# Optimization experiments

Measured on AMD Instinct MI355X. Metric: run time of the kernel, lower is better.

The kernel has to match this reference:

```python
import jax, jax.numpy as jnp
import numpy as np

NB_COMP = 8
LAT_DIM = 512
NB_NEUR = 1024
OUT_DIM = 512
N_SAMPLES = 16384


def setup_inputs() -> dict:
    key = jax.random.key(0)
    ks = jax.random.split(key, 8)
    s1 = 1.0 / np.sqrt(LAT_DIM)
    s2 = 1.0 / np.sqrt(NB_NEUR)
    return {
        "epsilon": jax.random.normal(ks[0], (N_SAMPLES, LAT_DIM), dtype=jnp.float32),
        "comp_idx": jax.random.randint(ks[1], (N_SAMPLES,), 0, NB_COMP, dtype=jnp.int32),
        "mu": jnp.zeros((NB_COMP, LAT_DIM), dtype=jnp.float32),
        "rho": jnp.zeros((NB_COMP,), dtype=jnp.float32),  # sigma = softplus(rho)
        "W1": jax.random.normal(ks[2], (NB_COMP, LAT_DIM, NB_NEUR), dtype=jnp.float32) * s1,
        "b1": jax.random.normal(ks[3], (NB_COMP, NB_NEUR), dtype=jnp.float32) * s1,
        "W2": jax.random.normal(ks[4], (NB_COMP, NB_NEUR, OUT_DIM), dtype=jnp.float32) * s2,
        "b2": jax.random.normal(ks[5], (NB_COMP, OUT_DIM), dtype=jnp.float32) * s2,
    }


def reference(epsilon, comp_idx, mu, rho, W1, b1, W2, b2):
    # GNNens.forward: per-sample categorical component dispatch through a
    # 1-hidden-layer sigmoid MLP. Vectorized as compute-all-components + select.
    sigma = jax.nn.softplus(rho)                          # [C]
    # lat_c[c,n,d] = epsilon[n,d] * sigma[c] + mu[c,d]
    lat = epsilon[None, :, :] * sigma[:, None, None] + mu[:, None, :]  # [C,N,D]
    h = jax.nn.sigmoid(jnp.einsum('cnd,cdh->cnh', lat, W1) + b1[:, None, :])  # [C,N,H]
    y = jnp.einsum('cnh,cho->cno', h, W2) + b2[:, None, :]                    # [C,N,O]
    # select each sample's routed component
    idx = comp_idx[None, :, None].astype(jnp.int32)       # [1,N,1]
    out = jnp.take_along_axis(y, idx, axis=0)[0]          # [N,O]
    return out
```

## Files before the change

kernel.cpp:

```cpp
#include <hip/hip_runtime.h>
#include <stdint.h>

#define NCOMP 8
#define LATD  512
#define HID   1024
#define OUTD  512
#define NS    16384

typedef unsigned short u16;
typedef __bf16 bf16x8 __attribute__((ext_vector_type(8)));
typedef float  f32x4  __attribute__((ext_vector_type(4)));

#define MAPS       (NS/128 + NCOMP)
#define SLOT_CHUNK ((MAPS + 7)/8)

#define ORDER_OFF  2048
#define APACK_OFF  (ORDER_OFF + NS*4)
#define W1T_OFF    (APACK_OFF + (size_t)NS*LATD*2)
#define W2T_OFF    (W1T_OFF + (size_t)NCOMP*LATD*HID*2)
#define H_OFF      (W2T_OFF + (size_t)NCOMP*HID*OUTD*2)
#define WS_NEEDED  (H_OFF + (size_t)NS*HID*2)

#define PACK_B0   8
#define PACK_NB   1024
#define W1T_B0    (PACK_B0 + PACK_NB)
#define W2T_B0    (W1T_B0 + 1024)
#define PREP_NB   (W2T_B0 + 1024)

#define G1_JOBS   (8*SLOT_CHUNK*(HID/128))
#define G2_JOBS   (8*SLOT_CHUNK*(OUTD/128))

__device__ __forceinline__ u16 f2b(float f) {
  unsigned int u = __builtin_bit_cast(unsigned int, f);
  u = (u + 0x7FFFu + ((u >> 16) & 1u)) >> 16;
  return (u16)u;
}

__device__ __forceinline__ unsigned pk2(float a, float b) {
  return (unsigned)f2b(a) | ((unsigned)f2b(b) << 16);
}

__device__ __forceinline__ void load_lds16(const void* g, void* l) {
  __builtin_amdgcn_global_load_lds((const __attribute__((address_space(1))) void*)g,
                                   (__attribute__((address_space(3))) void*)l, 16, 0, 0);
}

__device__ __forceinline__
void wtrans64(const float* __restrict__ src, u16* __restrict__ dst,
              int CC, int R, int c0, int r0, float* tile ) {
  const int t = threadIdx.x;
  const int tx4 = (t & 15) << 2;
  const int ty  = t >> 4;
  float4 v[4];
  #pragma unroll
  for (int r = 0; r < 4; ++r)
    v[r] = *reinterpret_cast<const float4*>(&src[(size_t)(r0 + ty + (r<<4))*CC + c0 + tx4]);
  #pragma unroll
  for (int r = 0; r < 4; ++r) {
    const int rr = ty + (r<<4);
    tile[rr*65 + tx4 + 0] = v[r].x;
    tile[rr*65 + tx4 + 1] = v[r].y;
    tile[rr*65 + tx4 + 2] = v[r].z;
    tile[rr*65 + tx4 + 3] = v[r].w;
  }
  __syncthreads();
  const int ch = t & 7;
  const int cc = t >> 3;
  #pragma unroll
  for (int q = 0; q < 2; ++q) {
    const int col = cc + (q << 5);
    uint4 o;
    o.x = pk2(tile[((ch<<3)+0)*65 + col], tile[((ch<<3)+1)*65 + col]);
    o.y = pk2(tile[((ch<<3)+2)*65 + col], tile[((ch<<3)+3)*65 + col]);
    o.z = pk2(tile[((ch<<3)+4)*65 + col], tile[((ch<<3)+5)*65 + col]);
    o.w = pk2(tile[((ch<<3)+6)*65 + col], tile[((ch<<3)+7)*65 + col]);
    *reinterpret_cast<uint4*>(&dst[(size_t)(c0+col)*R + r0 + (ch<<3)]) = o;
  }
}

__global__ __launch_bounds__(256)
void k_prep(const int* __restrict__ idx, const float* __restrict__ rho,
            const float* __restrict__ eps, const float* __restrict__ mu,
            const float* __restrict__ W1, const float* __restrict__ W2,
            int* __restrict__ offsets, int* __restrict__ ntiles,
            int* __restrict__ map, int* __restrict__ order,
            u16* __restrict__ Apack, u16* __restrict__ W1T, u16* __restrict__ W2T) {
  __shared__ float tile[64*65];
  __shared__ int hist_s[NCOMP];
  __shared__ int wtot[4];
  const int b = blockIdx.x;
  const int t = threadIdx.x;

  if (b < NCOMP) {
    const int c = b;
    const int wave = t >> 6, lane = t & 63;
    unsigned long long lo = 0, hi = 0;
    for (int i = 0; i < 64; ++i) {
      int v = idx[t + (i << 8)];
      unsigned long long one = 1ull << ((v & 3) << 4);
      if (v < 4) lo += one; else hi += one;
    }
    if (t < NCOMP) hist_s[t] = 0;
    __syncthreads();

    unsigned long long rlo = lo, rhi = hi;
    #pragma unroll
    for (int d = 1; d < 64; d <<= 1) { rlo += __shfl_xor(rlo, d); rhi += __shfl_xor(rhi, d); }
    if (lane == 0) {
      #pragma unroll
      for (int cc = 0; cc < 4; ++cc) atomicAdd(&hist_s[cc],   (int)((rlo >> (cc<<4)) & 0xffff));
      #pragma unroll
      for (int cc = 0; cc < 4; ++cc) atomicAdd(&hist_s[cc+4], (int)((rhi >> (cc<<4)) & 0xffff));
    }

    int v = (int)(((c < 4 ? lo : hi) >> ((c & 3) << 4)) & 0xffff);
    int s = v;
    #pragma unroll
    for (int d = 1; d < 64; d <<= 1) { int u = __shfl_up(s, d); if (lane >= d) s += u; }
    if (lane == 63) wtot[wave] = s;
    __syncthreads();

    int wbase = 0;
    for (int w = 0; w < wave; ++w) wbase += wtot[w];
    int off_c = 0;
    #pragma unroll
    for (int cc = 0; cc < NCOMP; ++cc) if (cc < c) off_c += hist_s[cc];

    int pos = off_c + wbase + (s - v);
    for (int i = 0; i < 64; ++i) {
      int smp = t + (i << 8);
      if (idx[smp] == c) order[pos++] = smp;
    }

    if (t == 0) {
      if (c == 0) {
        int a = 0;
        for (int cc = 0; cc < NCOMP; ++cc) { offsets[cc] = a; a += hist_s[cc]; }
        offsets[NCOMP] = a;
        int tot = 0;
        for (int cc = 0; cc < NCOMP; ++cc) tot += (hist_s[cc] + 127) >> 7;
        ntiles[0] = tot;
      }
      int mb = 0;
      for (int cc = 0; cc < c; ++cc) mb += (hist_s[cc] + 127) >> 7;
      int nt = (hist_s[c] + 127) >> 7;
      for (int m = 0; m < nt; ++m) map[mb + m] = (c << 16) | m;
    }
  } else if (b < W1T_B0) {
    const int wave = t >> 6, lane = t & 63;
    const int base = ((b - PACK_B0) << 4) + (wave << 1);
    const float4* eps4 = reinterpret_cast<const float4*>(eps);
    const float4* mu4  = reinterpret_cast<const float4*>(mu);
    uint2* ap2 = reinterpret_cast<uint2*>(Apack);
    #pragma unroll
    for (int it = 0; it < 2; ++it) {
      const int s0 = base + (it << 3);
      const int s1 = s0 + 1;
      int ca = idx[s0], cb = idx[s1];
      float ra = rho[ca], rb = rho[cb];
      float sga = (ra > 20.f) ? ra : log1pf(expf(ra));
      float sgb = (rb > 20.f) ? rb : log1pf(expf(rb));
      float4 ea0 = eps4[(size_t)s0*128 + lane];
      float4 ea1 = eps4[(size_t)s0*128 + 64 + lane];
      float4 eb0 = eps4[(size_t)s1*128 + lane];
      float4 eb1 = eps4[(size_t)s1*128 + 64 + lane];
      float4 ma0 = mu4[(size_t)ca*128 + lane];
      float4 ma1 = mu4[(size_t)ca*128 + 64 + lane];
      float4 mb0 = mu4[(size_t)cb*128 + lane];
      float4 mb1 = mu4[(size_t)cb*128 + 64 + lane];
      uint2 oa0, oa1, ob0, ob1;
      oa0.x = pk2(ea0.x*sga+ma0.x, ea0.y*sga+ma0.y);
      oa0.y = pk2(ea0.z*sga+ma0.z, ea0.w*sga+ma0.w);
      oa1.x = pk2(ea1.x*sga+ma1.x, ea1.y*sga+ma1.y);
      oa1.y = pk2(ea1.z*sga+ma1.z, ea1.w*sga+ma1.w);
      ob0.x = pk2(eb0.x*sgb+mb0.x, eb0.y*sgb+mb0.y);
      ob0.y = pk2(eb0.z*sgb+mb0.z, eb0.w*sgb+mb0.w);
      ob1.x = pk2(eb1.x*sgb+mb1.x, eb1.y*sgb+mb1.y);
      ob1.y = pk2(eb1.z*sgb+mb1.z, eb1.w*sgb+mb1.w);
      ap2[(size_t)s0*128 + lane]      = oa0;
      ap2[(size_t)s0*128 + 64 + lane] = oa1;
      ap2[(size_t)s1*128 + lane]      = ob0;
      ap2[(size_t)s1*128 + 64 + lane] = ob1;
    }
  } else if (b < W2T_B0) {
    int bb = b - W1T_B0;
    int comp = bb >> 7, loc = bb & 127;
    wtrans64(W1 + (size_t)comp*LATD*HID, W1T + (size_t)comp*LATD*HID,
             HID, LATD, (loc & 15) << 6, (loc >> 4) << 6, tile);
  } else {
    int bb = b - W2T_B0;
    int comp = bb >> 7, loc = bb & 127;
    wtrans64(W2 + (size_t)comp*HID*OUTD, W2T + (size_t)comp*HID*OUTD,
             OUTD, HID, (loc & 7) << 6, (loc >> 3) << 6, tile);
  }
}

template<int K, int NB, int STAGE>
__device__ __forceinline__
void gemm_tile(const int id, const u16* __restrict__ A, const u16* __restrict__ BT,
               const int* __restrict__ offsets, const int* __restrict__ ntiles,
               const int* __restrict__ map, const int* __restrict__ order,
               const float* __restrict__ bias,
               u16* __restrict__ Hout, float* __restrict__ Yout,
               u16* As, u16* Bs, int* ord) {
  constexpr int NCB = NB/128;
  const int xcd   = id & 7;
  const int sub   = id >> 3;
  const int ncolb = sub % NCB;
  const int slot  = xcd*SLOT_CHUNK + sub / NCB;
  if (slot >= ntiles[0]) return;
  const int packed = map[slot];
  const int c      = packed >> 16;
  const int bstart = offsets[c];
  const int bend   = offsets[c+1];
  const int tile0  = bstart + (packed & 0xffff)*128;
  const int ncol0  = ncolb*128;

  const int tid  = threadIdx.x;
  const int wave = tid >> 6;
  const int lane = tid & 63;
  const int srow = (wave<<5) + (lane>>3);
  const int scol = ((lane & 7) ^ ((lane >> 3) & 7)) << 3;

  if (STAGE == 2 && tid < 128) {
    int gr = tile0 + tid;
    ord[tid] = order[gr < bend ? gr : bstart];
  }

  size_t a_off[4], b_off[4];
  const size_t bbase = (size_t)c * NB * K;
  #pragma unroll
  for (int i = 0; i < 4; ++i) {
    int ar = tile0 + srow + (i<<3);
    if (ar >= bend) ar = bend - 1;
    int arow = (STAGE == 1) ? order[ar] : ar;
    a_off[i] = (size_t)arow * K + scol;
    b_off[i] = bbase + (size_t)(ncol0 + srow + (i<<3)) * K + scol;
  }

  const int wr   = (wave >> 1) << 6;
  const int wc   = (wave & 1) << 6;
  const int quad = lane >> 4;
  const int l16  = lane & 15;
  const int sw   = l16 & 7;

  f32x4 acc[4][4] = {};

  for (int k0 = 0; k0 < K; k0 += 64) {
    #pragma unroll
    for (int i = 0; i < 4; ++i)
      load_lds16(A + a_off[i] + k0, &As[((wave<<5) + (i<<3))<<6]);
    #pragma unroll
    for (int i = 0; i < 4; ++i)
      load_lds16(BT + b_off[i] + k0, &Bs[((wave<<5) + (i<<3))<<6]);
    __syncthreads();
    #pragma unroll
    for (int kk = 0; kk < 64; kk += 32) {
      const int kc = (kk >> 3) + quad;
      const int sc = (kc ^ sw) << 3;
      bf16x8 af[4], bfr[4];
      #pragma unroll
      for (int mi = 0; mi < 4; ++mi)
        af[mi] = *reinterpret_cast<const bf16x8*>(&As[((wr + (mi<<4) + l16)<<6) + sc]);
      #pragma unroll
      for (int ni = 0; ni < 4; ++ni)
        bfr[ni] = *reinterpret_cast<const bf16x8*>(&Bs[((wc + (ni<<4) + l16)<<6) + sc]);
      #pragma unroll
      for (int ni = 0; ni < 4; ++ni)
        #pragma unroll
        for (int mi = 0; mi < 4; ++mi)
          acc[ni][mi] = __builtin_amdgcn_mfma_f32_16x16x32_bf16(bfr[ni], af[mi], acc[ni][mi], 0, 0, 0);
    }
    __syncthreads();
  }

  f32x4 bias4[4];
  #pragma unroll
  for (int ni = 0; ni < 4; ++ni)
    bias4[ni] = *reinterpret_cast<const f32x4*>(
        &bias[(size_t)c*NB + ncol0 + wc + (ni<<4) + (quad<<2)]);

  #pragma unroll
  for (int mi = 0; mi < 4; ++mi) {
    const int row_l = wr + (mi<<4) + l16;
    const int grow  = tile0 + row_l;
    if (grow < bend) {
      #pragma unroll
      for (int ni = 0; ni < 4; ++ni) {
        const int col = ncol0 + wc + (ni<<4) + (quad<<2);
        float v0 = acc[ni][mi][0] + bias4[ni][0];
        float v1 = acc[ni][mi][1] + bias4[ni][1];
        float v2 = acc[ni][mi][2] + bias4[ni][2];
        float v3 = acc[ni][mi][3] + bias4[ni][3];
        if (STAGE == 1) {
          v0 = __builtin_amdgcn_rcpf(1.0f + __expf(-v0));
          v1 = __builtin_amdgcn_rcpf(1.0f + __expf(-v1));
          v2 = __builtin_amdgcn_rcpf(1.0f + __expf(-v2));
          v3 = __builtin_amdgcn_rcpf(1.0f + __expf(-v3));
          uint2 pk;
          pk.x = (unsigned)f2b(v0) | ((unsigned)f2b(v1) << 16);
          pk.y = (unsigned)f2b(v2) | ((unsigned)f2b(v3) << 16);
          *reinterpret_cast<uint2*>(&Hout[(size_t)grow*NB + col]) = pk;
        } else {
          float4 o; o.x = v0; o.y = v1; o.z = v2; o.w = v3;
          *reinterpret_cast<float4*>(&Yout[(size_t)ord[row_l]*NB + col]) = o;
        }
      }
    }
  }
}

__global__ __launch_bounds__(256, 4)
void k_gemm1(const u16* __restrict__ Apack, const u16* __restrict__ W1T,
             const int* __restrict__ offsets, const int* __restrict__ ntiles,
             const int* __restrict__ map, const int* __restrict__ order,
             const float* __restrict__ b1, u16* __restrict__ Hout) {
  __shared__ __attribute__((aligned(16))) u16 As[128*64];
  __shared__ __attribute__((aligned(16))) u16 Bs[128*64];
  __shared__ int ord[128];
  #pragma unroll
  for (int j = 0; j < 2; ++j) {
    const int id = blockIdx.x + (j << 10);
    if (id < G1_JOBS) {
      if (j) __syncthreads();
      gemm_tile<LATD, HID, 1>(id, Apack, W1T, offsets, ntiles, map, order, b1,
                              Hout, nullptr, As, Bs, ord);
    }
  }
}

__global__ __launch_bounds__(256, 4)
void k_gemm2(const u16* __restrict__ Hws, const u16* __restrict__ W2T,
             const int* __restrict__ offsets, const int* __restrict__ ntiles,
             const int* __restrict__ map, const int* __restrict__ order,
             const float* __restrict__ b2, float* __restrict__ Yout) {
  __shared__ __attribute__((aligned(16))) u16 As[128*64];
  __shared__ __attribute__((aligned(16))) u16 Bs[128*64];
  __shared__ int ord[128];
  gemm_tile<HID, OUTD, 2>(blockIdx.x, Hws, W2T, offsets, ntiles, map, order, b2,
                          nullptr, Yout, As, Bs, ord);
}

__global__ void k_naive(const float* __restrict__ eps, const int* __restrict__ idx,
                        const float* __restrict__ mu, const float* __restrict__ rho,
                        const float* __restrict__ W1, const float* __restrict__ b1,
                        const float* __restrict__ W2, const float* __restrict__ b2,
                        float* __restrict__ out) {
  __shared__ float lat[LATD];
  __shared__ float h[HID];
  int n = blockIdx.x, t = threadIdx.x;
  int c = idx[n];
  float r = rho[c];
  float sg = (r > 20.f) ? r : log1pf(expf(r));
  for (int d = t; d < LATD; d += 256) lat[d] = eps[(size_t)n*LATD+d]*sg + mu[(size_t)c*LATD+d];
  __syncthreads();
  for (int j = t; j < HID; j += 256) {
    float a = b1[(size_t)c*HID+j];
    const float* w = W1 + (size_t)c*LATD*HID + j;
    for (int d = 0; d < LATD; ++d) a += lat[d]*w[(size_t)d*HID];
    h[j] = 1.f/(1.f+expf(-a));
  }
  __syncthreads();
  for (int o = t; o < OUTD; o += 256) {
    float a = b2[(size_t)c*OUTD+o];
    const float* w = W2 + (size_t)c*HID*OUTD + o;
    for (int j = 0; j < HID; ++j) a += h[j]*w[(size_t)j*OUTD];
    out[(size_t)n*OUTD+o] = a;
  }
}

extern "C" void kernel_launch(void* const* d_in, const int* in_sizes, int n_in,
                              void* d_out, int out_size, void* d_ws, size_t ws_size,
                              hipStream_t stream) {
  const float* eps = (const float*)d_in[0];
  const int*   idx = (const int*)d_in[1];
  const float* mu  = (const float*)d_in[2];
  const float* rho = (const float*)d_in[3];
  const float* W1  = (const float*)d_in[4];
  const float* b1  = (const float*)d_in[5];
  const float* W2  = (const float*)d_in[6];
  const float* b2  = (const float*)d_in[7];
  float* out = (float*)d_out;

  if (ws_size < WS_NEEDED) {
    k_naive<<<NS, 256, 0, stream>>>(eps, idx, mu, rho, W1, b1, W2, b2, out);
    return;
  }

  char* ws = (char*)d_ws;
  int*   offsets = (int*)(ws + 0);
  int*   ntiles  = (int*)(ws + 96);
  int*   map     = (int*)(ws + 128);
  int*   order   = (int*)(ws + ORDER_OFF);
  u16*   Apack   = (u16*)(ws + APACK_OFF);
  u16*   W1T     = (u16*)(ws + W1T_OFF);
  u16*   W2T     = (u16*)(ws + W2T_OFF);
  u16*   Hws     = (u16*)(ws + H_OFF);

  k_prep<<<PREP_NB, 256, 0, stream>>>(
      idx, rho, eps, mu, W1, W2, offsets, ntiles, map, order, Apack, W1T, W2T);
  k_gemm1<<<1024, 256, 0, stream>>>(
      Apack, W1T, offsets, ntiles, map, order, b1, Hws);
  k_gemm2<<<G2_JOBS, 256, 0, stream>>>(
      Hws, W2T, offsets, ntiles, map, order, b2, out);
}
```

Before: 188.6 us.

## Double-buffer LDS tiles with K-step 32 to overlap loads and MFMA

```diff
diff --git a/kernel.cpp b/kernel.cpp
--- a/kernel.cpp
+++ b/kernel.cpp
@@ -219,59 +219,70 @@
   const int tid  = threadIdx.x;
   const int wave = tid >> 6;
   const int lane = tid & 63;
-  const int srow = (wave<<5) + (lane>>3);
-  const int scol = ((lane & 7) ^ ((lane >> 3) & 7)) << 3;
 
   if (STAGE == 2 && tid < 128) {
     int gr = tile0 + tid;
     ord[tid] = order[gr < bend ? gr : bstart];
   }
 
-  size_t a_off[4], b_off[4];
+  const int sr  = lane >> 2;
+  const int scs = (((lane & 3) ^ ((lane >> 3) & 3)) << 3);
+  size_t a_off[2], b_off[2];
+  int dst_e[2];
   const size_t bbase = (size_t)c * NB * K;
   #pragma unroll
-  for (int i = 0; i < 4; ++i) {
-    int ar = tile0 + srow + (i<<3);
+  for (int i = 0; i < 2; ++i) {
+    const int r = (wave<<5) + (i<<4) + sr;
+    int ar = tile0 + r;
     if (ar >= bend) ar = bend - 1;
     int arow = (STAGE == 1) ? order[ar] : ar;
-    a_off[i] = (size_t)arow * K + scol;
-    b_off[i] = bbase + (size_t)(ncol0 + srow + (i<<3)) * K + scol;
+    a_off[i] = (size_t)arow * K + scs;
+    b_off[i] = bbase + (size_t)(ncol0 + r) * K + scs;
+    dst_e[i] = ((wave<<5) + (i<<4)) << 5;
   }
 
   const int wr   = (wave >> 1) << 6;
   const int wc   = (wave & 1) << 6;
   const int quad = lane >> 4;
   const int l16  = lane & 15;
-  const int sw   = l16 & 7;
+  const int sc   = ((quad ^ ((l16 >> 1) & 3)) << 3);
 
   f32x4 acc[4][4] = {};
 
-  for (int k0 = 0; k0 < K; k0 += 64) {
-    #pragma unroll
-    for (int i = 0; i < 4; ++i)
-      load_lds16(A + a_off[i] + k0, &As[((wave<<5) + (i<<3))<<6]);
-    #pragma unroll
-    for (int i = 0; i < 4; ++i)
-      load_lds16(BT + b_off[i] + k0, &Bs[((wave<<5) + (i<<3))<<6]);
-    __syncthreads();
-    #pragma unroll
-    for (int kk = 0; kk < 64; kk += 32) {
-      const int kc = (kk >> 3) + quad;
-      const int sc = (kc ^ sw) << 3;
-      bf16x8 af[4], bfr[4];
+  #pragma unroll
+  for (int i = 0; i < 2; ++i) {
+    load_lds16(A  + a_off[i], &As[dst_e[i]]);
+    load_lds16(BT + b_off[i], &Bs[dst_e[i]]);
+  }
+  __syncthreads();
+
+  int buf = 0;
+  for (int t = 0; t < K/32; ++t) {
+    const int nk = (t + 1) << 5;
+    if (nk < K) {
+      const int nb = (buf ^ 1) << 12;
+      #pragma unroll
+      for (int i = 0; i < 2; ++i) {
+        load_lds16(A  + a_off[i] + nk, &As[nb + dst_e[i]]);
+        load_lds16(BT + b_off[i] + nk, &Bs[nb + dst_e[i]]);
+      }
+    }
+    const u16* Ab = &As[buf << 12];
+    const u16* Bb = &Bs[buf << 12];
+    bf16x8 af[4], bfr[4];
+    #pragma unroll
+    for (int mi = 0; mi < 4; ++mi)
+      af[mi] = *reinterpret_cast<const bf16x8*>(&Ab[((wr + (mi<<4) + l16)<<5) + sc]);
+    #pragma unroll
+    for (int ni = 0; ni < 4; ++ni)
+      bfr[ni] = *reinterpret_cast<const bf16x8*>(&Bb[((wc + (ni<<4) + l16)<<5) + sc]);
+    #pragma unroll
+    for (int ni = 0; ni < 4; ++ni)
       #pragma unroll
       for (int mi = 0; mi < 4; ++mi)
-        af[mi] = *reinterpret_cast<const bf16x8*>(&As[((wr + (mi<<4) + l16)<<6) + sc]);
-      #pragma unroll
-      for (int ni = 0; ni < 4; ++ni)
-        bfr[ni] = *reinterpret_cast<const bf16x8*>(&Bs[((wc + (ni<<4) + l16)<<6) + sc]);
-      #pragma unroll
-      for (int ni = 0; ni < 4; ++ni)
-        #pragma unroll
-        for (int mi = 0; mi < 4; ++mi)
-          acc[ni][mi] = __builtin_amdgcn_mfma_f32_16x16x32_bf16(bfr[ni], af[mi], acc[ni][mi], 0, 0, 0);
-    }
+        acc[ni][mi] = __builtin_amdgcn_mfma_f32_16x16x32_bf16(bfr[ni], af[mi], acc[ni][mi], 0, 0, 0);
     __syncthreads();
+    buf ^= 1;
   }
 
   f32x4 bias4[4];
@@ -315,8 +326,8 @@
              const int* __restrict__ offsets, const int* __restrict__ ntiles,
              const int* __restrict__ map, const int* __restrict__ order,
              const float* __restrict__ b1, u16* __restrict__ Hout) {
-  __shared__ __attribute__((aligned(16))) u16 As[128*64];
-  __shared__ __attribute__((aligned(16))) u16 Bs[128*64];
+  __shared__ __attribute__((aligned(16))) u16 As[2*128*32];
+  __shared__ __attribute__((aligned(16))) u16 Bs[2*128*32];
   __shared__ int ord[128];
   #pragma unroll
   for (int j = 0; j < 2; ++j) {
@@ -334,8 +345,8 @@
              const int* __restrict__ offsets, const int* __restrict__ ntiles,
              const int* __restrict__ map, const int* __restrict__ order,
              const float* __restrict__ b2, float* __restrict__ Yout) {
-  __shared__ __attribute__((aligned(16))) u16 As[128*64];
-  __shared__ __attribute__((aligned(16))) u16 Bs[128*64];
+  __shared__ __attribute__((aligned(16))) u16 As[2*128*32];
+  __shared__ __attribute__((aligned(16))) u16 Bs[2*128*32];
   __shared__ int ord[128];
   gemm_tile<HID, OUTD, 2>(blockIdx.x, Hws, W2T, offsets, ntiles, map, order, b2,
                           nullptr, Yout, As, Bs, ord);
```

Measured after the change: 208.4 us. +10.5%, slower.

## Fuse prep and both GEMMs into one cooperative kernel with grid syncs

Applied to the files above, without the earlier changes.

```diff
diff --git a/kernel.cpp b/kernel.cpp
--- a/kernel.cpp
+++ b/kernel.cpp
@@ -1,5 +1,8 @@
 #include <hip/hip_runtime.h>
+#include <hip/hip_cooperative_groups.h>
 #include <stdint.h>
+
+namespace cg = cooperative_groups;
 
 #define NCOMP 8
 #define LATD  512
@@ -29,6 +32,7 @@
 
 #define G1_JOBS   (8*SLOT_CHUNK*(HID/128))
 #define G2_JOBS   (8*SLOT_CHUNK*(OUTD/128))
+#define COOP_NB   1024
 
 __device__ __forceinline__ u16 f2b(float f) {
   unsigned int u = __builtin_bit_cast(unsigned int, f);
@@ -44,6 +48,11 @@
   __builtin_amdgcn_global_load_lds((const __attribute__((address_space(1))) void*)g,
                                    (__attribute__((address_space(3))) void*)l, 16, 0, 0);
 }
+
+union __attribute__((aligned(16))) PrepGemmSmem {
+  struct { u16 As[128*64]; u16 Bs[128*64]; } g;
+  struct { float tile[64*65]; int hist[NCOMP]; int wtot[4]; } p;
+};
 
 __device__ __forceinline__
 void wtrans64(const float* __restrict__ src, u16* __restrict__ dst,
@@ -78,21 +87,19 @@
   }
 }
 
-__global__ __launch_bounds__(256)
-void k_prep(const int* __restrict__ idx, const float* __restrict__ rho,
-            const float* __restrict__ eps, const float* __restrict__ mu,
-            const float* __restrict__ W1, const float* __restrict__ W2,
-            int* __restrict__ offsets, int* __restrict__ ntiles,
-            int* __restrict__ map, int* __restrict__ order,
-            u16* __restrict__ Apack, u16* __restrict__ W1T, u16* __restrict__ W2T) {
-  __shared__ float tile[64*65];
-  __shared__ int hist_s[NCOMP];
-  __shared__ int wtot[4];
-  const int b = blockIdx.x;
+__device__ __forceinline__
+void prep_job(int job, const int* __restrict__ idx, const float* __restrict__ rho,
+              const float* __restrict__ eps, const float* __restrict__ mu,
+              const float* __restrict__ W1, const float* __restrict__ W2,
+              int* __restrict__ offsets, int* __restrict__ ntiles,
+              int* __restrict__ map, int* __restrict__ order,
+              u16* __restrict__ Apack, u16* __restrict__ W1T, u16* __restrict__ W2T,
+              PrepGemmSmem* sm) {
   const int t = threadIdx.x;
-
-  if (b < NCOMP) {
-    const int c = b;
+  if (job < NCOMP) {
+    int* hist_s = sm->p.hist;
+    int* wtot   = sm->p.wtot;
+    const int c = job;
     const int wave = t >> 6, lane = t & 63;
     unsigned long long lo = 0, hi = 0;
     for (int i = 0; i < 64; ++i) {
@@ -146,9 +153,9 @@
       int nt = (hist_s[c] + 127) >> 7;
       for (int m = 0; m < nt; ++m) map[mb + m] = (c << 16) | m;
     }
-  } else if (b < W1T_B0) {
+  } else if (job < W1T_B0) {
     const int wave = t >> 6, lane = t & 63;
-    const int base = ((b - PACK_B0) << 4) + (wave << 1);
+    const int base = ((job - PACK_B0) << 4) + (wave << 1);
     const float4* eps4 = reinterpret_cast<const float4*>(eps);
     const float4* mu4  = reinterpret_cast<const float4*>(mu);
     uint2* ap2 = reinterpret_cast<uint2*>(Apack);
@@ -182,16 +189,16 @@
       ap2[(size_t)s1*128 + lane]      = ob0;
       ap2[(size_t)s1*128 + 64 + lane] = ob1;
     }
-  } else if (b < W2T_B0) {
-    int bb = b - W1T_B0;
+  } else if (job < W2T_B0) {
+    int bb = job - W1T_B0;
     int comp = bb >> 7, loc = bb & 127;
     wtrans64(W1 + (size_t)comp*LATD*HID, W1T + (size_t)comp*LATD*HID,
-             HID, LATD, (loc & 15) << 6, (loc >> 4) << 6, tile);
+             HID, LATD, (loc & 15) << 6, (loc >> 4) << 6, sm->p.tile);
   } else {
-    int bb = b - W2T_B0;
+    int bb = job - W2T_B0;
     int comp = bb >> 7, loc = bb & 127;
     wtrans64(W2 + (size_t)comp*HID*OUTD, W2T + (size_t)comp*HID*OUTD,
-             OUTD, HID, (loc & 7) << 6, (loc >> 3) << 6, tile);
+             OUTD, HID, (loc & 7) << 6, (loc >> 3) << 6, sm->p.tile);
   }
 }
 
@@ -311,6 +318,60 @@
 }
 
 __global__ __launch_bounds__(256, 4)
+void k_fused(const int* __restrict__ idx, const float* __restrict__ rho,
+             const float* __restrict__ eps, const float* __restrict__ mu,
+             const float* __restrict__ W1, const float* __restrict__ W2,
+             const float* __restrict__ b1, const float* __restrict__ b2,
+             int* __restrict__ offsets, int* __restrict__ ntiles,
+             int* __restrict__ map, int* __restrict__ order,
+             u16* __restrict__ Apack, u16* __restrict__ W1T, u16* __restrict__ W2T,
+             u16* __restrict__ Hws, float* __restrict__ out) {
+  __shared__ PrepGemmSmem sm;
+  __shared__ int ord[128];
+  const int b = blockIdx.x;
+  cg::grid_group grid = cg::this_grid();
+
+  #pragma unroll 1
+  for (int j = 0; j < 4; ++j) {
+    const int job = b + (j << 10);
+    if (job >= PREP_NB) break;
+    if (j) __syncthreads();
+    prep_job(job, idx, rho, eps, mu, W1, W2,
+             offsets, ntiles, map, order, Apack, W1T, W2T, &sm);
+  }
+  __threadfence();
+  grid.sync();
+
+  #pragma unroll 1
+  for (int j = 0; j < 2; ++j) {
+    const int id = b + (j << 10);
+    if (id < G1_JOBS) {
+      if (j) __syncthreads();
+      gemm_tile<LATD, HID, 1>(id, Apack, W1T, offsets, ntiles, map, order, b1,
+                              Hws, nullptr, sm.g.As, sm.g.Bs, ord);
+    }
+  }
+  __threadfence();
+  grid.sync();
+
+  if (b < G2_JOBS)
+    gemm_tile<HID, OUTD, 2>(b, Hws, W2T, offsets, ntiles, map, order, b2,
+                            nullptr, out, sm.g.As, sm.g.Bs, ord);
+}
+
+__global__ __launch_bounds__(256)
+void k_prep(const int* __restrict__ idx, const float* __restrict__ rho,
+            const float* __restrict__ eps, const float* __restrict__ mu,
+            const float* __restrict__ W1, const float* __restrict__ W2,
+            int* __restrict__ offsets, int* __restrict__ ntiles,
+            int* __restrict__ map, int* __restrict__ order,
+            u16* __restrict__ Apack, u16* __restrict__ W1T, u16* __restrict__ W2T) {
+  __shared__ PrepGemmSmem sm;
+  prep_job(blockIdx.x, idx, rho, eps, mu, W1, W2,
+           offsets, ntiles, map, order, Apack, W1T, W2T, &sm);
+}
+
+__global__ __launch_bounds__(256, 4)
 void k_gemm1(const u16* __restrict__ Apack, const u16* __restrict__ W1T,
              const int* __restrict__ offsets, const int* __restrict__ ntiles,
              const int* __restrict__ map, const int* __restrict__ order,
@@ -318,15 +379,8 @@
   __shared__ __attribute__((aligned(16))) u16 As[128*64];
   __shared__ __attribute__((aligned(16))) u16 Bs[128*64];
   __shared__ int ord[128];
-  #pragma unroll
-  for (int j = 0; j < 2; ++j) {
-    const int id = blockIdx.x + (j << 10);
-    if (id < G1_JOBS) {
-      if (j) __syncthreads();
-      gemm_tile<LATD, HID, 1>(id, Apack, W1T, offsets, ntiles, map, order, b1,
-                              Hout, nullptr, As, Bs, ord);
-    }
-  }
+  gemm_tile<LATD, HID, 1>(blockIdx.x, Apack, W1T, offsets, ntiles, map, order, b1,
+                          Hout, nullptr, As, Bs, ord);
 }
 
 __global__ __launch_bounds__(256, 4)
@@ -397,9 +451,20 @@
   u16*   W2T     = (u16*)(ws + W2T_OFF);
   u16*   Hws     = (u16*)(ws + H_OFF);
 
+  void* args[] = {
+    (void*)&idx, (void*)&rho, (void*)&eps, (void*)&mu,
+    (void*)&W1,  (void*)&W2,  (void*)&b1,  (void*)&b2,
+    (void*)&offsets, (void*)&ntiles, (void*)&map, (void*)&order,
+    (void*)&Apack, (void*)&W1T, (void*)&W2T, (void*)&Hws, (void*)&out
+  };
+  hipError_t e = hipLaunchCooperativeKernel((const void*)k_fused,
+                                            dim3(COOP_NB), dim3(256),
+                                            args, 0, stream);
+  if (e == hipSuccess) return;
+
   k_prep<<<PREP_NB, 256, 0, stream>>>(
       idx, rho, eps, mu, W1, W2, offsets, ntiles, map, order, Apack, W1T, W2T);
-  k_gemm1<<<1024, 256, 0, stream>>>(
+  k_gemm1<<<G1_JOBS, 256, 0, stream>>>(
       Apack, W1T, offsets, ntiles, map, order, b1, Hws);
   k_gemm2<<<G2_JOBS, 256, 0, stream>>>(
       Hws, W2T, offsets, ntiles, map, order, b2, out);
```

New measurement: 692.7 us. 3.67x slower.
